# Kernel optimization log

Hardware: AMD Instinct MI355X
Metric: run time of the kernel (lower is better)

## Reference

```python
import jax, jax.numpy as jnp
import numpy as np

NHEAD = 8  # nn.MultiheadAttention default in TransformerDecoderLayerOptimal
LN_EPS = 1e-5


def layer_norm(x, g, b):
    m = x.mean(-1, keepdims=True)
    v = ((x - m) ** 2).mean(-1, keepdims=True)
    return (x - m) * jax.lax.rsqrt(v + LN_EPS) * g + b


def setup_inputs() -> dict:
    key = jax.random.key(0)
    ks = jax.random.split(key, 16)
    B, S, F0, D, L, C, DF = 32, 1024, 2048, 768, 100, 1000, 10
    sc = 0.02
    return {
        "x": jax.random.normal(ks[0], (B, S, F0), jnp.float32),
        "y": jax.random.normal(ks[1], (L, D), jnp.float32),
        "embed_W": jax.random.normal(ks[2], (D, F0), jnp.float32) * sc,
        "embed_b": jnp.zeros((D,), jnp.float32),
        "Wq": jax.random.normal(ks[3], (D, D), jnp.float32) * sc,
        "Wk": jax.random.normal(ks[4], (D, D), jnp.float32) * sc,
        "Wv": jax.random.normal(ks[5], (D, D), jnp.float32) * sc,
        "bq": jnp.zeros((D,), jnp.float32),
        "bk": jnp.zeros((D,), jnp.float32),
        "bv": jnp.zeros((D,), jnp.float32),
        "Wo": jax.random.normal(ks[6], (D, D), jnp.float32) * sc,
        "bo": jnp.zeros((D,), jnp.float32),
        "ln1_g": jnp.ones((D,), jnp.float32), "ln1_b": jnp.zeros((D,), jnp.float32),
        "ln2_g": jnp.ones((D,), jnp.float32), "ln2_b": jnp.zeros((D,), jnp.float32),
        "ln3_g": jnp.ones((D,), jnp.float32), "ln3_b": jnp.zeros((D,), jnp.float32),
        "ffn_W1": jax.random.normal(ks[7], (D, D), jnp.float32) * sc,  # dim_feedforward = d_model
        "ffn_b1": jnp.zeros((D,), jnp.float32),
        "ffn_W2": jax.random.normal(ks[8], (D, D), jnp.float32) * sc,
        "ffn_b2": jnp.zeros((D,), jnp.float32),
        "dup_pool": jax.random.normal(ks[9], (L, 2 * D, DF), jnp.float32) * sc,
        "dup_bias": jnp.zeros((C,), jnp.float32),
    }


def reference(x, y, embed_W, embed_b, Wq, Wk, Wv, bq, bk, bv, Wo, bo,
              ln1_g, ln1_b, ln2_g, ln2_b, ln3_g, ln3_b,
              ffn_W1, ffn_b1, ffn_W2, ffn_b2, dup_pool, dup_bias):
    B = x.shape[0]
    L, D = y.shape
    H, hd = NHEAD, D // NHEAD
    num_classes = dup_bias.shape[0]

    # embed_standart + relu : (B,S,F0) -> (B,S,D)
    mem = jax.nn.relu(jnp.einsum('bsf,df->bsd', x, embed_W) + embed_b)

    # tgt = query_embed repeated over batch (batch-first here)
    tgt0 = jnp.broadcast_to(y[None], (B, L, D))

    # TransformerDecoderLayerOptimal (eval mode: dropout = identity)
    t = layer_norm(tgt0 + tgt0, ln1_g, ln1_b)  # tgt + dropout1(tgt)

    # cross multi-head attention
    q = (jnp.einsum('bld,ed->ble', t, Wq) + bq).reshape(B, L, H, hd)
    k = (jnp.einsum('bsd,ed->bse', mem, Wk) + bk).reshape(B, -1, H, hd)
    v = (jnp.einsum('bsd,ed->bse', mem, Wv) + bv).reshape(B, -1, H, hd)
    scores = jnp.einsum('blhe,bshe->bhls', q, k) / np.float32(np.sqrt(hd))
    attn = jax.nn.softmax(scores, axis=-1)           # (B,H,L,S)
    ao = jnp.einsum('bhls,bshe->blhe', attn, v).reshape(B, L, D)
    ao = jnp.einsum('bld,ed->ble', ao, Wo) + bo
    t = layer_norm(t + ao, ln2_g, ln2_b)

    # FFN
    f = jnp.einsum('bld,ed->ble',
                   jax.nn.relu(jnp.einsum('bld,ed->ble', t, ffn_W1) + ffn_b1),
                   ffn_W2) + ffn_b2
    h = layer_norm(t + f, ln3_g, ln3_b)              # (B,L,D)

    # concat label embedding after h, then GroupFC (per-label grouped matmul)
    hcat = jnp.concatenate([h, tgt0], axis=-1)       # (B,L,2D)
    out_extrap = jnp.einsum('bld,ldf->blf', hcat, dup_pool)  # (B,L,DF)
    logits = out_extrap.reshape(B, -1)[:, :num_classes] + dup_bias

    a_score = attn.mean(axis=1)                      # MHA averages heads: (B,L,S)
    return logits, a_score
```

## Files before the change

### kernel.cpp

```cpp
#include <hip/hip_runtime.h>

typedef unsigned short u16;
typedef __bf16 bf16x8 __attribute__((ext_vector_type(8)));
typedef short s16x8 __attribute__((ext_vector_type(8)));
typedef u16 u16x4 __attribute__((ext_vector_type(4)));
typedef float f32x4 __attribute__((ext_vector_type(4)));

__device__ __forceinline__ float b2f(u16 u) {
  union { unsigned u32; float f; } x; x.u32 = ((unsigned)u) << 16; return x.f;
}
__device__ __forceinline__ u16 f2b(float f) {
  union { float f; unsigned u; } x; x.f = f;
  unsigned r = x.u + 0x7fffu + ((x.u >> 16) & 1u);
  return (u16)(r >> 16);
}

template <int F32>
__device__ __forceinline__ s16x8 load8(const void* __restrict__ p, size_t idx) {
  if (F32) {
    const float* f = (const float*)p + idx;
    f32x4 a = *(const f32x4*)f;
    f32x4 b = *(const f32x4*)(f + 4);
    s16x8 r;
    r[0] = (short)f2b(a[0]); r[1] = (short)f2b(a[1]);
    r[2] = (short)f2b(a[2]); r[3] = (short)f2b(a[3]);
    r[4] = (short)f2b(b[0]); r[5] = (short)f2b(b[1]);
    r[6] = (short)f2b(b[2]); r[7] = (short)f2b(b[3]);
    return r;
  } else {
    return *(const s16x8*)((const u16*)p + idx);
  }
}

__device__ __forceinline__ void gl16(const u16* g, u16* l) {
  __builtin_amdgcn_global_load_lds(
      (const __attribute__((address_space(1))) void*)g,
      (__attribute__((address_space(3))) void*)l, 16, 0, 0);
}

__global__ __launch_bounds__(256) void cvt_kernel(const float* __restrict__ in,
                                                  u16* __restrict__ out, int n8) {
  int i = blockIdx.x * 256 + threadIdx.x;
  if (i < n8) *(s16x8*)&out[(size_t)i * 8] = load8<1>(in, (size_t)i * 8);
}

__global__ __launch_bounds__(256) void cvt3_kernel(
    const float* __restrict__ a, const float* __restrict__ b,
    const float* __restrict__ c, u16* __restrict__ oa, u16* __restrict__ ob,
    u16* __restrict__ oc, int n8) {
  int i = blockIdx.x * 256 + threadIdx.x;
  const float* in = blockIdx.y == 0 ? a : (blockIdx.y == 1 ? b : c);
  u16* out = blockIdx.y == 0 ? oa : (blockIdx.y == 1 ? ob : oc);
  if (i < n8) *(s16x8*)&out[(size_t)i * 8] = load8<1>(in, (size_t)i * 8);
}

template <int RELU, int AF32, int TRANSC>
__global__ __launch_bounds__(256) void gemm_bt_kernel(
    const void* __restrict__ A, const u16* __restrict__ Bt,
    const float* __restrict__ bias, u16* __restrict__ C,
    int M, int N, int K) {
  __shared__ u16 As[128][32];
  __shared__ u16 Bs[128][32];
  const int tid = threadIdx.x;
  const int lane = tid & 63;
  const int wave = tid >> 6;
  const int wm = wave >> 1, wn = wave & 1;
  const int nwg = gridDim.x;
  const int orig = blockIdx.x;
  const int q = nwg >> 3, r = nwg & 7;
  const int xcd = orig & 7, loc = orig >> 3;
  const int wgid = (xcd < r ? xcd * (q + 1) : r * (q + 1) + (xcd - r) * q) + loc;
  const int NT = N >> 7;
  const int tn = wgid % NT, tm = wgid / NT;
  const size_t abase = (size_t)tm * 128 * K;
  const size_t bbase = (size_t)tn * 128 * K;
  const int fr = lane & 15;
  const int fk = (lane >> 4) << 3;
  const int grow = lane >> 2;
  const int gkoff = (lane & 3) << 3;
  const u16* bgp = Bt + bbase + (size_t)(wave * 32 + grow) * K + gkoff;
  u16* lB0 = &Bs[wave * 32][0];
  u16* lB1 = &Bs[wave * 32 + 16][0];
  const u16* agp = nullptr;
  u16 *lA0 = nullptr, *lA1 = nullptr;
  if (!AF32) {
    agp = (const u16*)A + abase + (size_t)(wave * 32 + grow) * K + gkoff;
    lA0 = &As[wave * 32][0];
    lA1 = &As[wave * 32 + 16][0];
  }
  const int lr = tid >> 2;
  const int lk = (tid & 3) << 3;
  f32x4 acc[4][4] = {};

  for (int k0 = 0; k0 < K; k0 += 32) {
    if (AF32) {
      *(s16x8*)&As[lr][lk]      = load8<1>(A, abase + (size_t)lr * K + k0 + lk);
      *(s16x8*)&As[lr + 64][lk] = load8<1>(A, abase + (size_t)(lr + 64) * K + k0 + lk);
    } else {
      gl16(agp + k0, lA0);
      gl16(agp + k0 + (size_t)16 * K, lA1);
    }
    gl16(bgp + k0, lB0);
    gl16(bgp + k0 + (size_t)16 * K, lB1);
    __syncthreads();
    bf16x8 af[4], bfv[4];
#pragma unroll
    for (int i = 0; i < 4; ++i)
      af[i] = __builtin_bit_cast(bf16x8, *(const s16x8*)&As[wm * 64 + i * 16 + fr][fk]);
#pragma unroll
    for (int j = 0; j < 4; ++j)
      bfv[j] = __builtin_bit_cast(bf16x8, *(const s16x8*)&Bs[wn * 64 + j * 16 + fr][fk]);
#pragma unroll
    for (int i = 0; i < 4; ++i)
#pragma unroll
      for (int j = 0; j < 4; ++j)
        acc[i][j] = __builtin_amdgcn_mfma_f32_16x16x32_bf16(af[i], bfv[j], acc[i][j], 0, 0, 0);
    __syncthreads();
  }

  const int row0 = tm * 128 + wm * 64 + ((lane >> 4) << 2);
  const int col0 = tn * 128 + wn * 64 + fr;
  if (TRANSC) {
#pragma unroll
    for (int j = 0; j < 4; ++j) {
      const int col = col0 + j * 16;
      const float bv = bias[col];
#pragma unroll
      for (int i = 0; i < 4; ++i) {
        const int row = row0 + i * 16;
        u16x4 pk;
#pragma unroll
        for (int r2 = 0; r2 < 4; ++r2) {
          float v = acc[i][j][r2] + bv;
          if (RELU) v = fmaxf(v, 0.f);
          pk[r2] = f2b(v);
        }
        size_t idx = ((size_t)(row >> 10) * N + col) * 1024 + (row & 1023);
        *(u16x4*)&C[idx] = pk;
      }
    }
  } else {
#pragma unroll
    for (int j = 0; j < 4; ++j) {
      const int col = col0 + j * 16;
      const float bv = bias[col];
#pragma unroll
      for (int i = 0; i < 4; ++i) {
#pragma unroll
        for (int r2 = 0; r2 < 4; ++r2) {
          float v = acc[i][j][r2] + bv;
          if (RELU) v = fmaxf(v, 0.f);
          C[(size_t)(row0 + i * 16 + r2) * N + col] = f2b(v);
        }
      }
    }
  }
}

__device__ __forceinline__ void block_stats(float s, float s2, float* red, int tid,
                                            float& S, float& S2) {
#pragma unroll
  for (int o = 32; o > 0; o >>= 1) { s += __shfl_xor(s, o); s2 += __shfl_xor(s2, o); }
  if ((tid & 63) == 0) { red[tid >> 6] = s; red[4 + (tid >> 6)] = s2; }
  __syncthreads();
  S = red[0] + red[1] + red[2] + red[3];
  S2 = red[4] + red[5] + red[6] + red[7];
}

__global__ __launch_bounds__(256) void t_kernel(const float* __restrict__ y,
                                                const float* __restrict__ g,
                                                const float* __restrict__ bb,
                                                float* __restrict__ t) {
  const int l = blockIdx.x, tid = threadIdx.x;
  __shared__ float red[8];
  float xv[3], s = 0.f, s2 = 0.f;
#pragma unroll
  for (int i = 0; i < 3; ++i) {
    int e = tid + i * 256;
    float v = 2.f * y[(size_t)l * 768 + e];
    xv[i] = v; s += v; s2 += v * v;
  }
  float S, S2;
  block_stats(s, s2, red, tid, S, S2);
  float mean = S * (1.f / 768.f);
  float var = S2 * (1.f / 768.f) - mean * mean;
  float inv = rsqrtf(var + 1e-5f);
#pragma unroll
  for (int i = 0; i < 3; ++i) {
    int e = tid + i * 256;
    t[(size_t)l * 768 + e] = (xv[i] - mean) * inv * g[e] + bb[e];
  }
}

__global__ __launch_bounds__(256) void q_kernel(const float* __restrict__ t,
                                                const float* __restrict__ Wq,
                                                const float* __restrict__ bq,
                                                float* __restrict__ q) {
  const int l = blockIdx.x, tid = threadIdx.x;
  __shared__ __align__(16) float ts[768];
  for (int i = tid; i < 768; i += 256) ts[i] = t[(size_t)l * 768 + i];
  __syncthreads();
  for (int e = tid; e < 768; e += 256) {
    const float* wr = Wq + (size_t)e * 768;
    float acc = bq[e];
    for (int j = 0; j < 768; j += 4) {
      f32x4 wv = *(const f32x4*)&wr[j];
      f32x4 tv = *(const f32x4*)&ts[j];
      acc += wv[0] * tv[0] + wv[1] * tv[1] + wv[2] * tv[2] + wv[3] * tv[3];
    }
    q[(size_t)l * 768 + e] = acc;
  }
}

__global__ __launch_bounds__(256) void c2_kernel(const float* __restrict__ y,
                                                 const float* __restrict__ pool,
                                                 const float* __restrict__ dbias,
                                                 float* __restrict__ c2) {
  const int l = blockIdx.x, tid = threadIdx.x, lane = tid & 63, w = tid >> 6;
  for (int j = w; j < 10; j += 4) {
    float acc = 0.f;
    for (int d = lane; d < 768; d += 64)
      acc += y[(size_t)l * 768 + d] * pool[((size_t)l * 1536 + 768 + d) * 10 + j];
#pragma unroll
    for (int o = 32; o > 0; o >>= 1) acc += __shfl_xor(acc, o);
    if (lane == 0) c2[l * 10 + j] = acc + dbias[l * 10 + j];
  }
}

__global__ __launch_bounds__(512) void attn_kernel(
    const float* __restrict__ q,
    const u16* __restrict__ kmat,
    const u16* __restrict__ vt,
    u16* __restrict__ ao,
    float* __restrict__ ascore) {
  const int b = blockIdx.x;
  const int l0 = blockIdx.y * 13;
  __shared__ float sc[13][1028];
  __shared__ __align__(16) u16 qs[16][96];
  __shared__ float rinv[16];
  const int tid = threadIdx.x;
  const int lane = tid & 63;
  const int w = tid >> 6;
  const int fr = lane & 15;
  const int hi = lane >> 4;
  const int fk = hi << 3;
  const int sfr = (fr < 13) ? fr : 12;
  float areg[26];
#pragma unroll
  for (int j = 0; j < 26; ++j) areg[j] = 0.f;

  for (int h = 0; h < 8; ++h) {
    for (int i = tid; i < 192; i += 512) {
      int r = i / 12, c8 = (i % 12) * 8;
      int l = l0 + r;
      s16x8 v = {};
      if (r < 13 && l < 100) v = load8<1>(q, (size_t)l * 768 + h * 96 + c8);
      *(s16x8*)&qs[r][c8] = v;
    }
    __syncthreads();
    bf16x8 af[3];
#pragma unroll
    for (int kk = 0; kk < 3; ++kk)
      af[kk] = __builtin_bit_cast(bf16x8, *(const s16x8*)&qs[fr][kk * 32 + fk]);
    const u16* kbase = kmat + (size_t)(b * 1024 + w * 128 + fr) * 768 + h * 96 + fk;
#pragma unroll 2
    for (int nt = 0; nt < 8; ++nt) {
      f32x4 acc = {};
      const u16* kp = kbase + (size_t)nt * 16 * 768;
#pragma unroll
      for (int kk = 0; kk < 3; ++kk) {
        bf16x8 bf = __builtin_bit_cast(bf16x8, *(const s16x8*)(kp + kk * 32));
        acc = __builtin_amdgcn_mfma_f32_16x16x32_bf16(af[kk], bf, acc, 0, 0, 0);
      }
      const int s = w * 128 + nt * 16 + fr;
#pragma unroll
      for (int r = 0; r < 4; ++r) {
        int lr2 = hi * 4 + r;
        if (lr2 < 13) sc[lr2][s] = acc[r] * 0.10206207261596575f;
      }
    }
    __syncthreads();
    for (int r = w; r < 13; r += 8) {
      float m = -1e30f;
      for (int i = lane; i < 1024; i += 64) m = fmaxf(m, sc[r][i]);
#pragma unroll
      for (int o = 32; o > 0; o >>= 1) m = fmaxf(m, __shfl_xor(m, o));
      float sum = 0.f;
      for (int i = lane; i < 1024; i += 64) {
        float e = __expf(sc[r][i] - m);
        sc[r][i] = e; sum += e;
      }
#pragma unroll
      for (int o = 32; o > 0; o >>= 1) sum += __shfl_xor(sum, o);
      if (lane == 0) rinv[r] = 1.f / sum;
    }
    __syncthreads();
#pragma unroll
    for (int j = 0; j < 26; ++j) {
      int i = tid + j * 512;
      int r = i >> 10;
      areg[j] += sc[r][i & 1023] * rinv[r];
    }
    f32x4 pacc[6];
#pragma unroll
    for (int nt = 0; nt < 6; ++nt) pacc[nt] = (f32x4){0.f, 0.f, 0.f, 0.f};
    const u16* vbase = vt + (size_t)(b * 768 + h * 96 + fr) * 1024 + w * 128 + fk;
#pragma unroll 2
    for (int ks = 0; ks < 4; ++ks) {
      const float* sp = &sc[sfr][w * 128 + ks * 32 + fk];
      bf16x8 paf;
#pragma unroll
      for (int j2 = 0; j2 < 8; ++j2) paf[j2] = (__bf16)sp[j2];
#pragma unroll
      for (int nt = 0; nt < 6; ++nt) {
        bf16x8 vf = __builtin_bit_cast(bf16x8,
            *(const s16x8*)(vbase + (size_t)nt * 16 * 1024 + ks * 32));
        pacc[nt] = __builtin_amdgcn_mfma_f32_16x16x32_bf16(paf, vf, pacc[nt], 0, 0, 0);
      }
    }
    __syncthreads();
    float* red = &sc[0][0];
#pragma unroll
    for (int nt = 0; nt < 6; ++nt) {
#pragma unroll
      for (int r = 0; r < 4; ++r) {
        int lr2 = hi * 4 + r;
        if (lr2 < 13) red[(w * 13 + lr2) * 96 + nt * 16 + fr] = pacc[nt][r];
      }
    }
    __syncthreads();
    for (int i = tid; i < 1248; i += 512) {
      int lr2 = i / 96, d = i % 96;
      float s = 0.f;
#pragma unroll
      for (int w8 = 0; w8 < 8; ++w8) s += red[(w8 * 13 + lr2) * 96 + d];
      int l = l0 + lr2;
      if (l < 100) ao[(size_t)(b * 100 + l) * 768 + h * 96 + d] = f2b(s * rinv[lr2]);
    }
    __syncthreads();
  }
#pragma unroll
  for (int j = 0; j < 26; ++j) {
    int i = tid + j * 512;
    int r = i >> 10;
    int l = l0 + r;
    if (l < 100) ascore[(size_t)(b * 100 + l) * 1024 + (i & 1023)] = areg[j] * 0.125f;
  }
}

__global__ __launch_bounds__(256) void ln_kernel(
    const float* __restrict__ base, const u16* __restrict__ add,
    const float* __restrict__ g, const float* __restrict__ bb,
    float* __restrict__ outf, u16* __restrict__ outb, int base_per_l) {
  const int row = blockIdx.x, tid = threadIdx.x;
  __shared__ float red[8];
  const size_t boff = (size_t)(base_per_l ? (row % 100) : row) * 768;
  const size_t aoff = (size_t)row * 768;
  float xv[3], s = 0.f, s2 = 0.f;
#pragma unroll
  for (int i = 0; i < 3; ++i) {
    int e = tid + i * 256;
    float v = base[boff + e] + b2f(add[aoff + e]);
    xv[i] = v; s += v; s2 += v * v;
  }
  float S, S2;
  block_stats(s, s2, red, tid, S, S2);
  float mean = S * (1.f / 768.f);
  float var = S2 * (1.f / 768.f) - mean * mean;
  float inv = rsqrtf(var + 1e-5f);
#pragma unroll
  for (int i = 0; i < 3; ++i) {
    int e = tid + i * 256;
    float o = (xv[i] - mean) * inv * g[e] + bb[e];
    if (outf) outf[aoff + e] = o;
    if (outb) outb[aoff + e] = f2b(o);
  }
}

__global__ __launch_bounds__(256) void groupfc_kernel(
    const u16* __restrict__ h, const float* __restrict__ pool,
    const float* __restrict__ c2, float* __restrict__ logits) {
  const int l = blockIdx.x, tid = threadIdx.x;
  __shared__ float ps[768][10];
  for (int i = tid; i < 7680; i += 256) ps[i / 10][i % 10] = pool[(size_t)l * 15360 + i];
  __syncthreads();
  for (int idx = tid; idx < 320; idx += 256) {
    int bb = idx / 10, j = idx % 10;
    const u16* hr = h + (size_t)(bb * 100 + l) * 768;
    float acc = c2[l * 10 + j];
    for (int d0 = 0; d0 < 768; d0 += 8) {
      s16x8 hv = *(const s16x8*)&hr[d0];
#pragma unroll
      for (int e = 0; e < 8; ++e) acc += b2f((u16)hv[e]) * ps[d0 + e][j];
    }
    logits[bb * 1000 + l * 10 + j] = acc;
  }
}

extern "C" void kernel_launch(void* const* d_in, const int* in_sizes, int n_in,
                              void* d_out, int out_size, void* d_ws, size_t ws_size,
                              hipStream_t stream) {
  (void)in_sizes; (void)n_in; (void)out_size; (void)ws_size;
  const float* x      = (const float*)d_in[0];
  const float* y      = (const float*)d_in[1];
  const float* embedW = (const float*)d_in[2];
  const float* embedb = (const float*)d_in[3];
  const float* Wq     = (const float*)d_in[4];
  const float* Wk     = (const float*)d_in[5];
  const float* Wv     = (const float*)d_in[6];
  const float* bq     = (const float*)d_in[7];
  const float* bk     = (const float*)d_in[8];
  const float* bv     = (const float*)d_in[9];
  const float* Wo     = (const float*)d_in[10];
  const float* bo     = (const float*)d_in[11];
  const float* ln1g   = (const float*)d_in[12];
  const float* ln1b   = (const float*)d_in[13];
  const float* ln2g   = (const float*)d_in[14];
  const float* ln2b   = (const float*)d_in[15];
  const float* ln3g   = (const float*)d_in[16];
  const float* ln3b   = (const float*)d_in[17];
  const float* W1     = (const float*)d_in[18];
  const float* b1     = (const float*)d_in[19];
  const float* W2     = (const float*)d_in[20];
  const float* b2     = (const float*)d_in[21];
  const float* pool   = (const float*)d_in[22];
  const float* dbias  = (const float*)d_in[23];

  char* w = (char*)d_ws;
  u16* kws = (u16*)(w);
  u16* vt  = (u16*)(w + 50331648);
  char* R  = w + 100663296;
  u16*   mem = (u16*)R;
  u16*   ao  = (u16*)(R + 0);
  u16*   u1  = (u16*)(R + 4915200);
  u16*   t2b = (u16*)(R + 9830400);
  u16*   f1  = (u16*)(R + 14745600);
  u16*   f2  = (u16*)(R + 19660800);
  u16*   hb  = (u16*)(R + 24576000);
  float* t2f = (float*)(R + 29491200);
  float* tf  = (float*)(w + 150994944);
  float* qf  = (float*)(w + 150994944 + 307200);
  float* c2  = (float*)(w + 150994944 + 614400);
  u16* wbE = (u16*)(w + 50331648);
  u16* wbK = (u16*)(w + 50331648 + 3145728);
  u16* wbV = (u16*)(w + 150994944 + 1048576);
  u16* wbO = (u16*)(w + 0);
  u16* wb1 = (u16*)(w + 1179648);
  u16* wb2 = (u16*)(w + 2359296);

  float* logits = (float*)d_out;
  float* ascore = (float*)d_out + 32000;

  cvt_kernel<<<dim3(768), dim3(256), 0, stream>>>(embedW, wbE, 196608);
  cvt_kernel<<<dim3(288), dim3(256), 0, stream>>>(Wk, wbK, 73728);
  cvt_kernel<<<dim3(288), dim3(256), 0, stream>>>(Wv, wbV, 73728);
  t_kernel<<<dim3(100), dim3(256), 0, stream>>>(y, ln1g, ln1b, tf);
  q_kernel<<<dim3(100), dim3(256), 0, stream>>>(tf, Wq, bq, qf);
  c2_kernel<<<dim3(100), dim3(256), 0, stream>>>(y, pool, dbias, c2);

  gemm_bt_kernel<1, 1, 0><<<dim3(1536), dim3(256), 0, stream>>>(x, wbE, embedb, mem, 32768, 768, 2048);
  gemm_bt_kernel<0, 0, 0><<<dim3(1536), dim3(256), 0, stream>>>(mem, wbK, bk, kws, 32768, 768, 768);
  gemm_bt_kernel<0, 0, 1><<<dim3(1536), dim3(256), 0, stream>>>(mem, wbV, bv, vt, 32768, 768, 768);

  attn_kernel<<<dim3(32, 8), dim3(512), 0, stream>>>(qf, kws, vt, ao, ascore);

  cvt3_kernel<<<dim3(288, 3), dim3(256), 0, stream>>>(Wo, W1, W2, wbO, wb1, wb2, 73728);
  gemm_bt_kernel<0, 0, 0><<<dim3(150), dim3(256), 0, stream>>>(ao, wbO, bo, u1, 3200, 768, 768);
  ln_kernel<<<dim3(3200), dim3(256), 0, stream>>>(tf, u1, ln2g, ln2b, t2f, t2b, 1);
  gemm_bt_kernel<1, 0, 0><<<dim3(150), dim3(256), 0, stream>>>(t2b, wb1, b1, f1, 3200, 768, 768);
  gemm_bt_kernel<0, 0, 0><<<dim3(150), dim3(256), 0, stream>>>(f1, wb2, b2, f2, 3200, 768, 768);
  ln_kernel<<<dim3(3200), dim3(256), 0, stream>>>(t2f, f2, ln3g, ln3b, (float*)nullptr, hb, 0);
  groupfc_kernel<<<dim3(100), dim3(256), 0, stream>>>(hb, pool, c2, logits);
}
```

Before: 1.010 ms.

## Double-buffer GEMM LDS tiles with register prefetch of fp32 A operand

After: 980.1 us. -3.0%, faster.

```diff
diff --git a/kernel.cpp b/kernel.cpp
--- a/kernel.cpp
+++ b/kernel.cpp
@@ -10,23 +10,23 @@
   union { unsigned u32; float f; } x; x.u32 = ((unsigned)u) << 16; return x.f;
 }
 __device__ __forceinline__ u16 f2b(float f) {
-  union { float f; unsigned u; } x; x.f = f;
-  unsigned r = x.u + 0x7fffu + ((x.u >> 16) & 1u);
-  return (u16)(r >> 16);
+  return __builtin_bit_cast(u16, (__bf16)f);
+}
+__device__ __forceinline__ s16x8 cvt8(f32x4 a, f32x4 b) {
+  s16x8 r;
+#pragma unroll
+  for (int i = 0; i < 4; ++i) {
+    r[i]     = (short)f2b(a[i]);
+    r[i + 4] = (short)f2b(b[i]);
+  }
+  return r;
 }
 
 template <int F32>
 __device__ __forceinline__ s16x8 load8(const void* __restrict__ p, size_t idx) {
   if (F32) {
     const float* f = (const float*)p + idx;
-    f32x4 a = *(const f32x4*)f;
-    f32x4 b = *(const f32x4*)(f + 4);
-    s16x8 r;
-    r[0] = (short)f2b(a[0]); r[1] = (short)f2b(a[1]);
-    r[2] = (short)f2b(a[2]); r[3] = (short)f2b(a[3]);
-    r[4] = (short)f2b(b[0]); r[5] = (short)f2b(b[1]);
-    r[6] = (short)f2b(b[2]); r[7] = (short)f2b(b[3]);
-    return r;
+    return cvt8(*(const f32x4*)f, *(const f32x4*)(f + 4));
   } else {
     return *(const s16x8*)((const u16*)p + idx);
   }
@@ -59,8 +59,8 @@
     const void* __restrict__ A, const u16* __restrict__ Bt,
     const float* __restrict__ bias, u16* __restrict__ C,
     int M, int N, int K) {
-  __shared__ u16 As[128][32];
-  __shared__ u16 Bs[128][32];
+  __shared__ u16 As[2][128][32];
+  __shared__ u16 Bs[2][128][32];
   const int tid = threadIdx.x;
   const int lane = tid & 63;
   const int wave = tid >> 6;
@@ -79,43 +79,72 @@
   const int grow = lane >> 2;
   const int gkoff = (lane & 3) << 3;
   const u16* bgp = Bt + bbase + (size_t)(wave * 32 + grow) * K + gkoff;
-  u16* lB0 = &Bs[wave * 32][0];
-  u16* lB1 = &Bs[wave * 32 + 16][0];
-  const u16* agp = nullptr;
-  u16 *lA0 = nullptr, *lA1 = nullptr;
-  if (!AF32) {
-    agp = (const u16*)A + abase + (size_t)(wave * 32 + grow) * K + gkoff;
-    lA0 = &As[wave * 32][0];
-    lA1 = &As[wave * 32 + 16][0];
-  }
+  const u16* agp = (const u16*)A + abase + (size_t)(wave * 32 + grow) * K + gkoff;
   const int lr = tid >> 2;
   const int lk = (tid & 3) << 3;
+  const float* afp  = (const float*)A + abase + (size_t)lr * K + lk;
+  const float* afp2 = afp + (size_t)64 * K;
+  const int nk = K >> 5;
   f32x4 acc[4][4] = {};
-
-  for (int k0 = 0; k0 < K; k0 += 32) {
-    if (AF32) {
-      *(s16x8*)&As[lr][lk]      = load8<1>(A, abase + (size_t)lr * K + k0 + lk);
-      *(s16x8*)&As[lr + 64][lk] = load8<1>(A, abase + (size_t)(lr + 64) * K + k0 + lk);
+  f32x4 p0, p1, p2, p3;
+
+  if (AF32) {
+    p0 = *(const f32x4*)afp;  p1 = *(const f32x4*)(afp + 4);
+    p2 = *(const f32x4*)afp2; p3 = *(const f32x4*)(afp2 + 4);
+    *(s16x8*)&As[0][lr][lk]      = cvt8(p0, p1);
+    *(s16x8*)&As[0][lr + 64][lk] = cvt8(p2, p3);
+    const int k1 = (nk > 1) ? 32 : 0;
+    p0 = *(const f32x4*)(afp + k1);  p1 = *(const f32x4*)(afp + k1 + 4);
+    p2 = *(const f32x4*)(afp2 + k1); p3 = *(const f32x4*)(afp2 + k1 + 4);
+  } else {
+    gl16(agp, &As[0][wave * 32][0]);
+    gl16(agp + (size_t)16 * K, &As[0][wave * 32 + 16][0]);
+  }
+  gl16(bgp, &Bs[0][wave * 32][0]);
+  gl16(bgp + (size_t)16 * K, &Bs[0][wave * 32 + 16][0]);
+
+  int c = 0;
+  for (int t = 0; t < nk; ++t) {
+    const int nb = c ^ 1;
+    if (t + 1 < nk) {
+      if (AF32) {
+        *(s16x8*)&As[nb][lr][lk]      = cvt8(p0, p1);
+        *(s16x8*)&As[nb][lr + 64][lk] = cvt8(p2, p3);
+        const int k2 = ((t + 2 < nk) ? (t + 2) : (nk - 1)) << 5;
+        p0 = *(const f32x4*)(afp + k2);  p1 = *(const f32x4*)(afp + k2 + 4);
+        p2 = *(const f32x4*)(afp2 + k2); p3 = *(const f32x4*)(afp2 + k2 + 4);
+      } else {
+        gl16(agp + (t + 1) * 32, &As[nb][wave * 32][0]);
+        gl16(agp + (t + 1) * 32 + (size_t)16 * K, &As[nb][wave * 32 + 16][0]);
+      }
+      gl16(bgp + (t + 1) * 32, &Bs[nb][wave * 32][0]);
+      gl16(bgp + (t + 1) * 32 + (size_t)16 * K, &Bs[nb][wave * 32 + 16][0]);
+    }
+    __builtin_amdgcn_sched_barrier(0);
+    if (t + 1 < nk) {
+      asm volatile("s_waitcnt vmcnt(%0)" ::"n"(AF32 ? 6 : 4) : "memory");
     } else {
-      gl16(agp + k0, lA0);
-      gl16(agp + k0 + (size_t)16 * K, lA1);
-    }
-    gl16(bgp + k0, lB0);
-    gl16(bgp + k0 + (size_t)16 * K, lB1);
-    __syncthreads();
+      asm volatile("s_waitcnt vmcnt(0)" ::: "memory");
+    }
+    if (AF32) asm volatile("s_waitcnt lgkmcnt(0)" ::: "memory");
+    __builtin_amdgcn_sched_barrier(0);
+    __builtin_amdgcn_s_barrier();
+    __builtin_amdgcn_sched_barrier(0);
+
     bf16x8 af[4], bfv[4];
 #pragma unroll
     for (int i = 0; i < 4; ++i)
-      af[i] = __builtin_bit_cast(bf16x8, *(const s16x8*)&As[wm * 64 + i * 16 + fr][fk]);
+      af[i] = __builtin_bit_cast(bf16x8, *(const s16x8*)&As[c][wm * 64 + i * 16 + fr][fk]);
 #pragma unroll
     for (int j = 0; j < 4; ++j)
-      bfv[j] = __builtin_bit_cast(bf16x8, *(const s16x8*)&Bs[wn * 64 + j * 16 + fr][fk]);
+      bfv[j] = __builtin_bit_cast(bf16x8, *(const s16x8*)&Bs[c][wn * 64 + j * 16 + fr][fk]);
 #pragma unroll
     for (int i = 0; i < 4; ++i)
 #pragma unroll
       for (int j = 0; j < 4; ++j)
         acc[i][j] = __builtin_amdgcn_mfma_f32_16x16x32_bf16(af[i], bfv[j], acc[i][j], 0, 0, 0);
-    __syncthreads();
+    __builtin_amdgcn_s_barrier();
+    c = nb;
   }
 
   const int row0 = tm * 128 + wm * 64 + ((lane >> 4) << 2);
```
